# Optimization experiments

Hardware: AMD Instinct MI355X
Metric: run time of the kernel (lower is better)

The kernel has to match this reference:

```python
import jax, jax.numpy as jnp
import numpy as np

B, N, K = 4, 2048, 32
H, DS, DE = 128, 128, 128
NUM_IN = DS + DE + H  # 384
SCALE = 30.0
EPS = 1e-5


def setup_inputs() -> dict:
    key = jax.random.key(0)
    ks = jax.random.split(key, 9)
    s = 0.05
    return {
        "h_S": jax.random.normal(ks[0], (B, N, DS), jnp.float32),
        "h_V": jax.random.normal(ks[1], (B, N, H), jnp.float32),
        "h_E": jax.random.normal(ks[2], (B, N, K, DE), jnp.float32),
        "E_idx": jax.random.randint(ks[3], (B, N, K), 0, N, jnp.int64),
        "mask_attend": jnp.ones((B, N, K), jnp.float32),
        "W1_w": jax.random.normal(ks[4], (H + NUM_IN, H), jnp.float32) * s,
        "W1_b": jnp.zeros((H,), jnp.float32),
        "W2_w": jax.random.normal(ks[5], (H, H), jnp.float32) * s,
        "W2_b": jnp.zeros((H,), jnp.float32),
        "ln_g": jnp.ones((H,), jnp.float32),
        "ln_b": jnp.zeros((H,), jnp.float32),
    }


def gather_nodes(nodes, idx):
    # nodes: [B, N, D], idx: [B, N, K] -> [B, N, K, D]
    b, n, k = idx.shape
    d = nodes.shape[-1]
    flat = jnp.broadcast_to(idx.reshape(b, n * k, 1), (b, n * k, d))
    return jnp.take_along_axis(nodes, flat, axis=1).reshape(b, n, k, d)


def layer_norm(x, g, b):
    mu = jnp.mean(x, axis=-1, keepdims=True)
    var = jnp.var(x, axis=-1, keepdims=True)
    return (x - mu) * jax.lax.rsqrt(var + EPS) * g + b


def reference(h_S, h_V, h_E, E_idx, mask_attend, W1_w, W1_b, W2_w, W2_b, ln_g, ln_b):
    # h_ES = cat(h_E, gather(h_S))  -> [B,N,K,DE+DS]
    h_ES = jnp.concatenate([h_E, gather_nodes(h_S, E_idx)], axis=-1)
    # h_EXV = cat(h_ES, gather(h_V)) -> [B,N,K,DE+DS+H], masked
    h_EXV = jnp.concatenate([h_ES, gather_nodes(h_V, E_idx)], axis=-1)
    h_EXV = mask_attend[..., None] * h_EXV
    # h_EV = cat(h_V expanded, h_EXV) -> [B,N,K,H+NUM_IN]
    h_V_exp = jnp.broadcast_to(h_V[:, :, None, :], (h_V.shape[0], h_V.shape[1], K, h_V.shape[2]))
    h_EV = jnp.concatenate([h_V_exp, h_EXV], axis=-1)
    # per-edge 2-layer MLP (exact GELU as torch.nn.GELU)
    h = jax.nn.gelu(jnp.einsum("bnkf,fh->bnkh", h_EV, W1_w) + W1_b, approximate=False)
    h_message = jnp.einsum("bnkh,hg->bnkg", h, W2_w) + W2_b
    dh = jnp.sum(h_message, axis=-2) / SCALE
    # dropout is identity in eval mode
    return layer_norm(h_V + dh, ln_g, ln_b)
```

## Files before the change

### kernel.cpp

```cpp
#include <hip/hip_runtime.h>
#include <math.h>

typedef float f32x4 __attribute__((ext_vector_type(4)));
typedef short s16x8 __attribute__((ext_vector_type(8)));
typedef unsigned u32x4 __attribute__((ext_vector_type(4)));

#define N_NODES 2048
#define KEDGE 32
#define HDIM 128
#define SB() __builtin_amdgcn_sched_barrier(0)

__device__ __forceinline__ short f2bf(float f){
  unsigned u = __builtin_bit_cast(unsigned, f);
  u += 0x7fffu + ((u >> 16) & 1u);
  return (short)(u >> 16);
}
__device__ __forceinline__ float bf2f(short s){
  unsigned u = ((unsigned)(unsigned short)s) << 16;
  return __builtin_bit_cast(float, u);
}
__device__ __forceinline__ unsigned cvt_pk_bf16(float a, float b){
  unsigned r;
  asm("v_cvt_pk_bf16_f32 %0, %1, %2" : "=v"(r) : "v"(a), "v"(b));
  return r;
}
__device__ __forceinline__ float fast_gelu(float x){
  float t = x * (-2.3022078f - 0.1029527f * x * x);
  float e = __builtin_amdgcn_exp2f(t);
  return x * __builtin_amdgcn_rcpf(1.0f + e);
}
__device__ __forceinline__ void gld16(const void* g, void* l){
  __builtin_amdgcn_global_load_lds(
      (const __attribute__((address_space(1))) void*)g,
      (__attribute__((address_space(3))) void*)l, 16, 0, 0);
}
__device__ __forceinline__ f32x4 mfma16(s16x8 a, s16x8 b, f32x4 c){
  return __builtin_amdgcn_mfma_f32_16x16x32_bf16(a, b, c, 0, 0, 0);
}

__global__ void prep1(const float* __restrict__ W1, const float* __restrict__ W2,
                      short* __restrict__ W1f, short* __restrict__ W2f,
                      unsigned* __restrict__ flag){
  if (blockIdx.x == 320){
    if (threadIdx.x == 0) *flag = 0u;
    return;
  }
  int t = blockIdx.x * 256 + threadIdx.x;
  if (t < 65536){
    int ks = t >> 12, r = t & 4095;
    int ct = r >> 9;  r &= 511;
    int lane = r >> 3, j = r & 7;
    int k = ks*32 + (lane>>4)*8 + j;
    int n = ct*16 + (lane&15);
    W1f[t] = f2bf(W1[k*128 + n]);
  } else if (t < 81920){
    int t2 = t - 65536;
    int ks = t2 >> 12, r = t2 & 4095;
    int ct = r >> 9;  r &= 511;
    int lane = r >> 3, j = r & 7;
    int k = ks*32 + (lane>>4)*8 + j;
    int n = ct*16 + (lane&15);
    W2f[t2] = f2bf(W2[k*128 + n]);
  }
}

__global__ __launch_bounds__(256)
void prep2(const float* __restrict__ hS, const float* __restrict__ hV,
           const float* __restrict__ b1, const short* __restrict__ W1f,
           short* __restrict__ Zb, short* __restrict__ Ub,
           const unsigned* __restrict__ Ei_u, unsigned* __restrict__ flag){
  if (blockIdx.x >= 128){
    int t = ((int)blockIdx.x - 128)*256 + threadIdx.x;
    unsigned v = Ei_u[2*t + 1];
    unsigned long long m = __ballot(v != 0u);
    if ((threadIdx.x & 63) == 0 && m) atomicOr(flag, 1u);
    return;
  }
  const int tid = threadIdx.x;
  const int w = tid >> 6, lane = tid & 63, l15 = lane & 15, lg = lane >> 4;
  const int nb = ((int)blockIdx.x*4 + w)*16;

  f32x4 accz[8], accu[8];
  #pragma unroll
  for (int ct = 0; ct < 8; ++ct){ accz[ct] = (f32x4){0,0,0,0}; accu[ct] = (f32x4){0,0,0,0}; }

  #pragma unroll
  for (int ks = 0; ks < 4; ++ks){
    const float* p = hS + (long)(nb + l15)*128 + ks*32 + lg*8;
    float4 x = *(const float4*)p, y = *(const float4*)(p + 4);
    u32x4 pk;
    pk[0] = cvt_pk_bf16(x.x, x.y); pk[1] = cvt_pk_bf16(x.z, x.w);
    pk[2] = cvt_pk_bf16(y.x, y.y); pk[3] = cvt_pk_bf16(y.z, y.w);
    s16x8 a = __builtin_bit_cast(s16x8, pk);
    #pragma unroll
    for (int ct = 0; ct < 8; ++ct){
      s16x8 bf = *(const s16x8*)(W1f + (8+ks)*4096 + ct*512 + lane*8);
      accz[ct] = mfma16(a, bf, accz[ct]);
    }
  }
  #pragma unroll
  for (int ks = 0; ks < 4; ++ks){
    const float* p = hV + (long)(nb + l15)*128 + ks*32 + lg*8;
    float4 x = *(const float4*)p, y = *(const float4*)(p + 4);
    u32x4 pk;
    pk[0] = cvt_pk_bf16(x.x, x.y); pk[1] = cvt_pk_bf16(x.z, x.w);
    pk[2] = cvt_pk_bf16(y.x, y.y); pk[3] = cvt_pk_bf16(y.z, y.w);
    s16x8 a = __builtin_bit_cast(s16x8, pk);
    #pragma unroll
    for (int ct = 0; ct < 8; ++ct){
      s16x8 bfd = *(const s16x8*)(W1f + (12+ks)*4096 + ct*512 + lane*8);
      accz[ct] = mfma16(a, bfd, accz[ct]);
      s16x8 bfa = *(const s16x8*)(W1f + (0+ks)*4096 + ct*512 + lane*8);
      accu[ct] = mfma16(a, bfa, accu[ct]);
    }
  }

  float b1v[8];
  #pragma unroll
  for (int ct = 0; ct < 8; ++ct) b1v[ct] = b1[ct*16 + l15];

  #pragma unroll
  for (int ct = 0; ct < 8; ++ct)
    #pragma unroll
    for (int i = 0; i < 4; ++i){
      const long row = nb + lg*4 + i;
      Zb[row*128 + ct*16 + l15] = f2bf(accz[ct][i]);
      Ub[row*128 + l15*8 + ct]  = f2bf(accu[ct][i] + b1v[ct]);
    }
}

__global__ __launch_bounds__(512)
void fusedF(const float* __restrict__ hE, const int* __restrict__ Eidx,
            const float* __restrict__ mask, const short* __restrict__ W1f,
            const short* __restrict__ Zb, const short* __restrict__ Ub,
            const unsigned* __restrict__ idx_flag, short* __restrict__ vb)
{
  __shared__ __align__(16) char smem[163840];

  const int tid  = threadIdx.x;
  const int w    = tid >> 6;
  const int lane = tid & 63;
  const int l15  = lane & 15;
  const int lg   = lane >> 4;

  const int n0 = ((int)blockIdx.x * 8 + w) * 4;
  const long zrow0 = (long)(n0 >> 11) * N_NODES;
  char* mybuf = smem + w*16384;
  const char* W1L = smem + 131072;

  const int rr = lane >> 5;
  const unsigned t0 = (unsigned)((rr << 9) | (((lane & 31) << 4) ^ (rr << 4)));

  #pragma unroll
  for (int q = 0; q < 4; ++q)
    gld16((const char*)W1f + 32768 + w*4096 + q*1024 + lane*16,
          smem + 131072 + w*4096 + q*1024);
  asm volatile("s_waitcnt vmcnt(0)" ::: "memory");
  SB();
  __builtin_amdgcn_s_barrier();

  s16x8 ifr[2];
  #pragma unroll
  for (int c2 = 0; c2 < 2; ++c2){
    const int active = ((lg >> 1) == c2);
    const int j = l15 - 8*(lg & 1);
    s16x8 f;
    #pragma unroll
    for (int e = 0; e < 8; ++e)
      f[e] = (active && j == e) ? (short)0x3F80 : (short)0;
    ifr[c2] = f;
  }

  const int is64 = (*idx_flag == 0u) ? 1 : 0;

  int e0, eZ;
  {
    const int ea = n0*32 + l15;
    const int eb = n0*32 + 16 + l15;
    e0 = Eidx[ea << is64];
    eZ = Eidx[eb << is64];
  }
  float maskC = mask[n0*32 + l15];
  s16x8 ubC = *(const s16x8*)(Ub + (long)n0*128 + l15*8);
  SB();
  #pragma unroll
  for (int q = 0; q < 8; ++q){
    const unsigned off = (unsigned)(q*1024) | (t0 ^ (unsigned)((2*q & 6) << 4));
    gld16((const char*)hE + (size_t)n0*16384 + off, mybuf + q*1024);
  }
  SB();
  s16x8 zbC[4];
  #pragma unroll
  for (int ks = 0; ks < 4; ++ks)
    zbC[ks] = *(const s16x8*)(Zb + (zrow0 + e0)*128 + ks*32 + lg*8);
  SB();

  float vacc[8];
  #pragma unroll
  for (int ct = 0; ct < 8; ++ct) vacc[ct] = 0.f;

  #pragma unroll 2
  for (int t = 0; t < 8; ++t){
    const int tn = (t+1) & 7;
    const int t2 = (t+2) & 7;
    const int nn_n = n0 + (tn >> 1);
    SB();
    float maskN = mask[nn_n*32 + (tn&1)*16 + l15];
    s16x8 ubN = *(const s16x8*)(Ub + (long)nn_n*128 + l15*8);
    const int eN = Eidx[((n0 + (t2>>1))*32 + (t2&1)*16 + l15) << is64];
    SB();
    {
      const size_t eb = (size_t)nn_n*16384 + (size_t)(tn&1)*8192;
      char* sbuf = mybuf + (tn&1)*8192;
      #pragma unroll
      for (int q = 0; q < 8; ++q){
        const unsigned off = (unsigned)(q*1024) | (t0 ^ (unsigned)((2*q & 6) << 4));
        gld16((const char*)hE + eb + off, sbuf + q*1024);
      }
    }
    SB();
    s16x8 zbN[4];
    #pragma unroll
    for (int ks = 0; ks < 4; ++ks)
      zbN[ks] = *(const s16x8*)(Zb + (zrow0 + eZ)*128 + ks*32 + lg*8);
    SB();
    if (t == 0 || (t & 1)) asm volatile("s_waitcnt vmcnt(15)" ::: "memory");
    else                   asm volatile("s_waitcnt vmcnt(23)" ::: "memory");
    SB();

    f32x4 acc1[8];
    #pragma unroll
    for (int ct = 0; ct < 8; ++ct) acc1[ct] = (f32x4){0,0,0,0};

    const char* cbuf = mybuf + (t&1)*8192;
    const int sw = (l15 & 7) << 4;
    const int rowb = l15 * 512;
    #pragma unroll
    for (int ks = 0; ks < 4; ++ks){
      const int c0 = ks*128 + lg*32;
      float4 ex = *(const float4*)(cbuf + rowb + (c0 ^ sw));
      float4 ey = *(const float4*)(cbuf + rowb + ((c0 + 16) ^ sw));
      u32x4 pk;
      pk[0] = cvt_pk_bf16(ex.x, ex.y); pk[1] = cvt_pk_bf16(ex.z, ex.w);
      pk[2] = cvt_pk_bf16(ey.x, ey.y); pk[3] = cvt_pk_bf16(ey.z, ey.w);
      s16x8 a = __builtin_bit_cast(s16x8, pk);
      const char* bb = W1L + ks*8192 + lane*16;
      #pragma unroll
      for (int ct = 0; ct < 8; ++ct){
        s16x8 bf = *(const s16x8*)(bb + ct*1024);
        acc1[ct] = mfma16(a, bf, acc1[ct]);
      }
      #pragma unroll
      for (int c2 = 0; c2 < 2; ++c2)
        acc1[ks*2 + c2] = mfma16(zbC[ks], ifr[c2], acc1[ks*2 + c2]);
    }

    float uv[8];
    #pragma unroll
    for (int ct = 0; ct < 8; ++ct) uv[ct] = bf2f(ubC[ct]);
    float mi[4];
    #pragma unroll
    for (int i = 0; i < 4; ++i) mi[i] = __shfl(maskC, lg*4 + i, 64);
    #pragma unroll
    for (int ct = 0; ct < 8; ++ct)
      #pragma unroll
      for (int i = 0; i < 4; ++i)
        vacc[ct] += fast_gelu(uv[ct] + mi[i]*acc1[ct][i]);

    if (t & 1){
      const long nn = n0 + (t >> 1);
      float v8[8];
      #pragma unroll
      for (int ct = 0; ct < 8; ++ct){
        float s = vacc[ct];
        s += __shfl_xor(s, 16, 64);
        s += __shfl_xor(s, 32, 64);
        v8[ct] = s;
        vacc[ct] = 0.f;
      }
      if (lg == 0){
        #pragma unroll
        for (int ct = 0; ct < 8; ++ct)
          vb[nn*128 + ct*16 + l15] = f2bf(v8[ct]);
      }
    }

    maskC = maskN; ubC = ubN; eZ = eN;
    #pragma unroll
    for (int ks = 0; ks < 4; ++ks) zbC[ks] = zbN[ks];
  }
}

__global__ __launch_bounds__(256, 4)
void pass3(const short* __restrict__ vb, const float* __restrict__ hV,
           const short* __restrict__ W2f, const float* __restrict__ W2b,
           const float* __restrict__ lng, const float* __restrict__ lnb,
           float* __restrict__ out)
{
  const int tid = threadIdx.x;
  const int w = tid >> 6, lane = tid & 63, l15 = lane & 15, lg = lane >> 4;
  const long m = (long)blockIdx.x*4 + w;

  s16x8 av[4];
  #pragma unroll
  for (int ks2 = 0; ks2 < 4; ++ks2)
    av[ks2] = *(const s16x8*)(vb + m*128 + ks2*32 + lg*8);

  f32x4 acc2[8];
  #pragma unroll
  for (int ct = 0; ct < 8; ++ct) acc2[ct] = (f32x4){0,0,0,0};
  #pragma unroll
  for (int ks2 = 0; ks2 < 4; ++ks2){
    const short* wb = W2f + ks2*4096 + lane*8;
    #pragma unroll
    for (int ct = 0; ct < 8; ++ct){
      s16x8 bf = *(const s16x8*)(wb + ct*512);
      acc2[ct] = mfma16(av[ks2], bf, acc2[ct]);
    }
  }

  float res[8], vs = 0.f, vq = 0.f;
  #pragma unroll
  for (int ct = 0; ct < 8; ++ct){
    const int c = ct*16 + l15;
    float dh  = (acc2[ct][0] + 32.0f * W2b[c]) * (1.0f/30.0f);
    float val = hV[m*128 + c] + dh;
    res[ct] = val;
    vs += val; vq += val*val;
  }
  vs += __shfl_xor(vs, 1, 64);  vs += __shfl_xor(vs, 2, 64);
  vs += __shfl_xor(vs, 4, 64);  vs += __shfl_xor(vs, 8, 64);
  vq += __shfl_xor(vq, 1, 64);  vq += __shfl_xor(vq, 2, 64);
  vq += __shfl_xor(vq, 4, 64);  vq += __shfl_xor(vq, 8, 64);
  const float mu  = vs * (1.0f/128.0f);
  const float var = vq * (1.0f/128.0f) - mu*mu;
  const float rs  = rsqrtf(var + 1e-5f);

  #pragma unroll
  for (int q = 0; q < 2; ++q){
    const int ct = lg*2 + q;
    const int c  = ct*16 + l15;
    out[m*128 + c] = (res[ct] - mu) * rs * lng[c] + lnb[c];
  }
}

extern "C" void kernel_launch(void* const* d_in, const int* in_sizes, int n_in,
                              void* d_out, int out_size, void* d_ws, size_t ws_size,
                              hipStream_t stream) {
  const float* hS  = (const float*)d_in[0];
  const float* hV  = (const float*)d_in[1];
  const float* hE  = (const float*)d_in[2];
  const int*   Ei  = (const int*)d_in[3];
  const float* mk  = (const float*)d_in[4];
  const float* W1w = (const float*)d_in[5];
  const float* W1b = (const float*)d_in[6];
  const float* W2w = (const float*)d_in[7];
  const float* W2b = (const float*)d_in[8];
  const float* lng = (const float*)d_in[9];
  const float* lnb = (const float*)d_in[10];

  short* W1f = (short*)d_ws;
  short* W2f = W1f + 65536;
  unsigned* flag = (unsigned*)((char*)d_ws + 163840);
  short* Zb = (short*)((char*)d_ws + 164096);
  short* Ub = (short*)((char*)d_ws + 2261248);
  short* vb = (short*)((char*)d_ws + 4358400);

  prep1<<<321, 256, 0, stream>>>(W1w, W2w, W1f, W2f, flag);
  prep2<<<640, 256, 0, stream>>>(hS, hV, W1b, W1f, Zb, Ub, (const unsigned*)Ei, flag);
  fusedF<<<256, 512, 0, stream>>>(hE, Ei, mk, W1f, Zb, Ub, flag, vb);
  pass3<<<2048, 256, 0, stream>>>(vb, hV, W2f, W2b, lng, lnb, (float*)d_out);
}
```

Baseline: 92.05 us.

## Fuse W2 projection and LayerNorm into edge kernel, keep W1 in registers

Measured after the change: 155.8 us. 69.2% more time.

```diff
diff --git a/kernel.cpp b/kernel.cpp
--- a/kernel.cpp
+++ b/kernel.cpp
@@ -67,7 +67,7 @@
 __global__ __launch_bounds__(256)
 void prep2(const float* __restrict__ hS, const float* __restrict__ hV,
            const float* __restrict__ b1, const short* __restrict__ W1f,
-           short* __restrict__ Zb, short* __restrict__ Ub,
+           short* __restrict__ Zb, unsigned* __restrict__ UHb,
            const unsigned* __restrict__ Ei_u, unsigned* __restrict__ flag){
   if (blockIdx.x >= 128){
     int t = ((int)blockIdx.x - 128)*256 + threadIdx.x;
@@ -125,15 +125,19 @@
     for (int i = 0; i < 4; ++i){
       const long row = nb + lg*4 + i;
       Zb[row*128 + ct*16 + l15] = f2bf(accz[ct][i]);
-      Ub[row*128 + l15*8 + ct]  = f2bf(accu[ct][i] + b1v[ct]);
+      unsigned u16 = (unsigned)(unsigned short)f2bf(accu[ct][i] + b1v[ct]);
+      unsigned h16 = (unsigned)(unsigned short)f2bf(hV[row*128 + ct*16 + l15]);
+      UHb[row*128 + l15*8 + ct] = u16 | (h16 << 16);
     }
 }
 
 __global__ __launch_bounds__(512)
 void fusedF(const float* __restrict__ hE, const int* __restrict__ Eidx,
             const float* __restrict__ mask, const short* __restrict__ W1f,
-            const short* __restrict__ Zb, const short* __restrict__ Ub,
-            const unsigned* __restrict__ idx_flag, short* __restrict__ vb)
+            const short* __restrict__ W2f, const short* __restrict__ Zb,
+            const unsigned* __restrict__ UHb, const unsigned* __restrict__ idx_flag,
+            const float* __restrict__ W2b, const float* __restrict__ lng,
+            const float* __restrict__ lnb, float* __restrict__ out)
 {
   __shared__ __align__(16) char smem[163840];
 
@@ -146,18 +150,32 @@
   const int n0 = ((int)blockIdx.x * 8 + w) * 4;
   const long zrow0 = (long)(n0 >> 11) * N_NODES;
   char* mybuf = smem + w*16384;
-  const char* W1L = smem + 131072;
+  const char* W2L = smem + 131072;
 
   const int rr = lane >> 5;
   const unsigned t0 = (unsigned)((rr << 9) | (((lane & 31) << 4) ^ (rr << 4)));
 
+  s16x8 wf[4][8];
+  #pragma unroll
+  for (int ks = 0; ks < 4; ++ks)
+    #pragma unroll
+    for (int ct = 0; ct < 8; ++ct)
+      wf[ks][ct] = *(const s16x8*)(W1f + (4+ks)*4096 + ct*512 + lane*8);
+  SB();
   #pragma unroll
   for (int q = 0; q < 4; ++q)
-    gld16((const char*)W1f + 32768 + w*4096 + q*1024 + lane*16,
+    gld16((const char*)W2f + w*4096 + q*1024 + lane*16,
           smem + 131072 + w*4096 + q*1024);
-  asm volatile("s_waitcnt vmcnt(0)" ::: "memory");
-  SB();
-  __builtin_amdgcn_s_barrier();
+  SB();
+
+  float w2b8[8], lngv[2], lnbv[2];
+  #pragma unroll
+  for (int ct = 0; ct < 8; ++ct) w2b8[ct] = W2b[ct*16 + l15];
+  #pragma unroll
+  for (int q = 0; q < 2; ++q){
+    const int c = (lg*2 + q)*16 + l15;
+    lngv[q] = lng[c]; lnbv[q] = lnb[c];
+  }
 
   s16x8 ifr[2];
   #pragma unroll
@@ -181,7 +199,9 @@
     eZ = Eidx[eb << is64];
   }
   float maskC = mask[n0*32 + l15];
-  s16x8 ubC = *(const s16x8*)(Ub + (long)n0*128 + l15*8);
+  s16x8 uhC[2];
+  uhC[0] = *(const s16x8*)((const short*)UHb + (long)n0*256 + l15*16);
+  uhC[1] = *(const s16x8*)((const short*)UHb + (long)n0*256 + l15*16 + 8);
   SB();
   #pragma unroll
   for (int q = 0; q < 8; ++q){
@@ -194,6 +214,9 @@
   for (int ks = 0; ks < 4; ++ks)
     zbC[ks] = *(const s16x8*)(Zb + (zrow0 + e0)*128 + ks*32 + lg*8);
   SB();
+  asm volatile("s_waitcnt vmcnt(0)" ::: "memory");
+  SB();
+  __builtin_amdgcn_s_barrier();
 
   float vacc[8];
   #pragma unroll
@@ -206,7 +229,9 @@
     const int nn_n = n0 + (tn >> 1);
     SB();
     float maskN = mask[nn_n*32 + (tn&1)*16 + l15];
-    s16x8 ubN = *(const s16x8*)(Ub + (long)nn_n*128 + l15*8);
+    s16x8 uhN[2];
+    uhN[0] = *(const s16x8*)((const short*)UHb + (long)nn_n*256 + l15*16);
+    uhN[1] = *(const s16x8*)((const short*)UHb + (long)nn_n*256 + l15*16 + 8);
     const int eN = Eidx[((n0 + (t2>>1))*32 + (t2&1)*16 + l15) << is64];
     SB();
     {
@@ -224,8 +249,8 @@
     for (int ks = 0; ks < 4; ++ks)
       zbN[ks] = *(const s16x8*)(Zb + (zrow0 + eZ)*128 + ks*32 + lg*8);
     SB();
-    if (t == 0 || (t & 1)) asm volatile("s_waitcnt vmcnt(15)" ::: "memory");
-    else                   asm volatile("s_waitcnt vmcnt(23)" ::: "memory");
+    if (t == 0 || (t & 1)) asm volatile("s_waitcnt vmcnt(16)" ::: "memory");
+    else                   asm volatile("s_waitcnt vmcnt(18)" ::: "memory");
     SB();
 
     f32x4 acc1[8];
@@ -244,12 +269,9 @@
       pk[0] = cvt_pk_bf16(ex.x, ex.y); pk[1] = cvt_pk_bf16(ex.z, ex.w);
       pk[2] = cvt_pk_bf16(ey.x, ey.y); pk[3] = cvt_pk_bf16(ey.z, ey.w);
       s16x8 a = __builtin_bit_cast(s16x8, pk);
-      const char* bb = W1L + ks*8192 + lane*16;
-      #pragma unroll
-      for (int ct = 0; ct < 8; ++ct){
-        s16x8 bf = *(const s16x8*)(bb + ct*1024);
-        acc1[ct] = mfma16(a, bf, acc1[ct]);
-      }
+      #pragma unroll
+      for (int ct = 0; ct < 8; ++ct)
+        acc1[ct] = mfma16(a, wf[ks][ct], acc1[ct]);
       #pragma unroll
       for (int c2 = 0; c2 < 2; ++c2)
         acc1[ks*2 + c2] = mfma16(zbC[ks], ifr[c2], acc1[ks*2 + c2]);
@@ -257,7 +279,7 @@
 
     float uv[8];
     #pragma unroll
-    for (int ct = 0; ct < 8; ++ct) uv[ct] = bf2f(ubC[ct]);
+    for (int ct = 0; ct < 4; ++ct){ uv[ct] = bf2f(uhC[0][2*ct]); uv[4+ct] = bf2f(uhC[1][2*ct]); }
     float mi[4];
     #pragma unroll
     for (int i = 0; i < 4; ++i) mi[i] = __shfl(maskC, lg*4 + i, 64);
@@ -268,7 +290,6 @@
         vacc[ct] += fast_gelu(uv[ct] + mi[i]*acc1[ct][i]);
 
     if (t & 1){
-      const long nn = n0 + (t >> 1);
       float v8[8];
       #pragma unroll
       for (int ct = 0; ct < 8; ++ct){
@@ -278,69 +299,60 @@
         v8[ct] = s;
         vacc[ct] = 0.f;
       }
-      if (lg == 0){
+      SB();
+      short* vl = (short*)(mybuf + (t&1)*8192);
+      #pragma unroll
+      for (int q = 0; q < 2; ++q){
+        const int ct = lg*2 + q;
+        vl[ct*16 + l15] = f2bf(v8[ct]);
+      }
+      asm volatile("s_waitcnt lgkmcnt(0)" ::: "memory");
+      SB();
+
+      f32x4 acc2[8];
+      #pragma unroll
+      for (int ct = 0; ct < 8; ++ct) acc2[ct] = (f32x4){0,0,0,0};
+      #pragma unroll
+      for (int ks2 = 0; ks2 < 4; ++ks2){
+        s16x8 av = *(const s16x8*)(vl + ks2*32 + lg*8);
+        const char* wb2 = W2L + ks2*8192 + lane*16;
         #pragma unroll
-        for (int ct = 0; ct < 8; ++ct)
-          vb[nn*128 + ct*16 + l15] = f2bf(v8[ct]);
-      }
-    }
-
-    maskC = maskN; ubC = ubN; eZ = eN;
+        for (int ct = 0; ct < 8; ++ct){
+          s16x8 bf = *(const s16x8*)(wb2 + ct*1024);
+          acc2[ct] = mfma16(av, bf, acc2[ct]);
+        }
+      }
+
+      float hv[8];
+      #pragma unroll
+      for (int ct = 0; ct < 4; ++ct){ hv[ct] = bf2f(uhC[0][2*ct+1]); hv[4+ct] = bf2f(uhC[1][2*ct+1]); }
+      float res[8], vs = 0.f, vq = 0.f;
+      #pragma unroll
+      for (int ct = 0; ct < 8; ++ct){
+        float dh  = (acc2[ct][0] + 32.0f * w2b8[ct]) * (1.0f/30.0f);
+        float val = hv[ct] + dh;
+        res[ct] = val;
+        vs += val; vq += val*val;
+      }
+      vs += __shfl_xor(vs, 1, 64);  vs += __shfl_xor(vs, 2, 64);
+      vs += __shfl_xor(vs, 4, 64);  vs += __shfl_xor(vs, 8, 64);
+      vq += __shfl_xor(vq, 1, 64);  vq += __shfl_xor(vq, 2, 64);
+      vq += __shfl_xor(vq, 4, 64);  vq += __shfl_xor(vq, 8, 64);
+      const float mu  = vs * (1.0f/128.0f);
+      const float var = vq * (1.0f/128.0f) - mu*mu;
+      const float rs  = rsqrtf(var + 1e-5f);
+
+      const long nodeoff = (long)(n0 + (t >> 1)) * HDIM;
+      #pragma unroll
+      for (int q = 0; q < 2; ++q){
+        const int ct = lg*2 + q;
+        out[nodeoff + ct*16 + l15] = (res[ct] - mu) * rs * lngv[q] + lnbv[q];
+      }
+    }
+
+    maskC = maskN; uhC[0] = uhN[0]; uhC[1] = uhN[1]; eZ = eN;
     #pragma unroll
     for (int ks = 0; ks < 4; ++ks) zbC[ks] = zbN[ks];
-  }
-}
-
-__global__ __launch_bounds__(256, 4)
-void pass3(const short* __restrict__ vb, const float* __restrict__ hV,
-           const short* __restrict__ W2f, const float* __restrict__ W2b,
-           const float* __restrict__ lng, const float* __restrict__ lnb,
-           float* __restrict__ out)
-{
-  const int tid = threadIdx.x;
-  const int w = tid >> 6, lane = tid & 63, l15 = lane & 15, lg = lane >> 4;
-  const long m = (long)blockIdx.x*4 + w;
-
-  s16x8 av[4];
-  #pragma unroll
-  for (int ks2 = 0; ks2 < 4; ++ks2)
-    av[ks2] = *(const s16x8*)(vb + m*128 + ks2*32 + lg*8);
-
-  f32x4 acc2[8];
-  #pragma unroll
-  for (int ct = 0; ct < 8; ++ct) acc2[ct] = (f32x4){0,0,0,0};
-  #pragma unroll
-  for (int ks2 = 0; ks2 < 4; ++ks2){
-    const short* wb = W2f + ks2*4096 + lane*8;
-    #pragma unroll
-    for (int ct = 0; ct < 8; ++ct){
-      s16x8 bf = *(const s16x8*)(wb + ct*512);
-      acc2[ct] = mfma16(av[ks2], bf, acc2[ct]);
-    }
-  }
-
-  float res[8], vs = 0.f, vq = 0.f;
-  #pragma unroll
-  for (int ct = 0; ct < 8; ++ct){
-    const int c = ct*16 + l15;
-    float dh  = (acc2[ct][0] + 32.0f * W2b[c]) * (1.0f/30.0f);
-    float val = hV[m*128 + c] + dh;
-    res[ct] = val;
-    vs += val; vq += val*val;
-  }
-  vs += __shfl_xor(vs, 1, 64);  vs += __shfl_xor(vs, 2, 64);
-  vs += __shfl_xor(vs, 4, 64);  vs += __shfl_xor(vs, 8, 64);
-  vq += __shfl_xor(vq, 1, 64);  vq += __shfl_xor(vq, 2, 64);
-  vq += __shfl_xor(vq, 4, 64);  vq += __shfl_xor(vq, 8, 64);
-  const float mu  = vs * (1.0f/128.0f);
-  const float var = vq * (1.0f/128.0f) - mu*mu;
-  const float rs  = rsqrtf(var + 1e-5f);
-
-  #pragma unroll
-  for (int q = 0; q < 2; ++q){
-    const int ct = lg*2 + q;
-    const int c  = ct*16 + l15;
-    out[m*128 + c] = (res[ct] - mu) * rs * lng[c] + lnb[c];
   }
 }
 
@@ -363,11 +375,10 @@
   short* W2f = W1f + 65536;
   unsigned* flag = (unsigned*)((char*)d_ws + 163840);
   short* Zb = (short*)((char*)d_ws + 164096);
-  short* Ub = (short*)((char*)d_ws + 2261248);
-  short* vb = (short*)((char*)d_ws + 4358400);
+  unsigned* UHb = (unsigned*)((char*)d_ws + 2261248);
 
   prep1<<<321, 256, 0, stream>>>(W1w, W2w, W1f, W2f, flag);
-  prep2<<<640, 256, 0, stream>>>(hS, hV, W1b, W1f, Zb, Ub, (const unsigned*)Ei, flag);
-  fusedF<<<256, 512, 0, stream>>>(hE, Ei, mk, W1f, Zb, Ub, flag, vb);
-  pass3<<<2048, 256, 0, stream>>>(vb, hV, W2f, W2b, lng, lnb, (float*)d_out);
-}
+  prep2<<<640, 256, 0, stream>>>(hS, hV, W1b, W1f, Zb, UHb, (const unsigned*)Ei, flag);
+  fusedF<<<256, 512, 0, stream>>>(hE, Ei, mk, W1f, W2f, Zb, UHb, flag,
+                                  W2b, lng, lnb, (float*)d_out);
+}
```
